# Optimization experiments

Measured on AMD Instinct MI355X. Metric: run time of the kernel, lower is better.

## Reference

```python
import jax, jax.numpy as jnp
import numpy as np

N_WIRES = 3  # state vector of 2^3 = 8 amplitudes, kept as [B,2,2,2]


def _rx(t):
    c = jnp.cos(t / 2); s = jnp.sin(t / 2)
    return jnp.stack([jnp.stack([c + 0j, -1j * s], -1),
                      jnp.stack([-1j * s, c + 0j], -1)], -2).astype(jnp.complex64)


def _ry(t):
    c = jnp.cos(t / 2); s = jnp.sin(t / 2)
    return jnp.stack([jnp.stack([c, -s], -1),
                      jnp.stack([s, c], -1)], -2).astype(jnp.complex64)


def _rz(t):
    e = jnp.exp(-1j * t / 2).astype(jnp.complex64)
    z = jnp.zeros_like(e)
    return jnp.stack([jnp.stack([e, z], -1),
                      jnp.stack([z, jnp.conj(e)], -1)], -2)


def apply_1q(state, mat, wire):
    # state: [B,2,2,2]; mat: [2,2] (shared) or [B,2,2] (per-sample)
    s = jnp.moveaxis(state, 1 + wire, 1)
    sh = s.shape
    s = s.reshape(sh[0], 2, -1)
    m = jnp.broadcast_to(mat, (sh[0], 2, 2))
    s = jnp.einsum('bij,bjk->bik', m, s)
    return jnp.moveaxis(s.reshape(sh), 1, 1 + wire)


def apply_crx(state, t, ctrl, tgt):
    # controlled-RX: apply rx(t) to target subspace where control bit == 1
    mat = _rx(t)  # [2,2]
    s = jnp.moveaxis(state, (1 + ctrl, 1 + tgt), (1, 2))  # [B,2(ctrl),2(tgt),2]
    s1 = s[:, 1]                       # [B,2,2]
    sh = s1.shape
    s1 = jnp.einsum('ij,bjk->bik', mat, s1.reshape(sh[0], 2, -1)).reshape(sh)
    s = jnp.stack([s[:, 0], s1], 1)
    return jnp.moveaxis(s, (1, 2), (1 + ctrl, 1 + tgt))


def _quantum_forward(x, theta, W1, b1, W2, b2):
    B = x.shape[0]
    state = jnp.zeros((B, 2, 2, 2), jnp.complex64).at[:, 0, 0, 0].set(1.0)
    # GeneralEncoder: rx(x0)@w0, ry(x1)@w1, rz(x2)@w2
    state = apply_1q(state, _rx(x[:, 0]), 0)
    state = apply_1q(state, _ry(x[:, 1]), 1)
    state = apply_1q(state, _rz(x[:, 2]), 2)
    # RandomLayer(n_ops=8): fixed representative 8-op trainable sequence
    state = apply_1q(state, _rx(theta[0]), 0)
    state = apply_1q(state, _ry(theta[1]), 1)
    state = apply_1q(state, _rz(theta[2]), 2)
    state = apply_crx(state, theta[3], 0, 1)
    state = apply_1q(state, _ry(theta[4]), 2)
    state = apply_1q(state, _rx(theta[5]), 1)
    state = apply_crx(state, theta[6], 1, 2)
    state = apply_1q(state, _rz(theta[7]), 0)
    # measurement -> 8 basis-state probabilities (matches Linear(8,32) head)
    probs = (state.real ** 2 + state.imag ** 2).reshape(B, 8)
    h = jax.nn.relu(probs @ W1 + b1)
    return h @ W2 + b2


def setup_inputs() -> dict:
    key = jax.random.key(0)
    ks = jax.random.split(key, 6)
    B = 2_000_000
    x = jax.random.normal(ks[0], (B, 3), jnp.float32)
    theta = jax.random.normal(ks[1], (8,), jnp.float32)
    W1 = jax.random.normal(ks[2], (8, 32), jnp.float32) * 0.35   # ~1/sqrt(8)
    b1 = jnp.zeros((32,), jnp.float32)
    W2 = jax.random.normal(ks[3], (32, 2), jnp.float32) * 0.18   # ~1/sqrt(32)
    b2 = jnp.zeros((2,), jnp.float32)
    return {"x": x, "theta": theta, "W1": W1, "b1": b1, "W2": W2, "b2": b2}


def reference(x, theta, W1, b1, W2, b2):
    return _quantum_forward(x, theta, W1, b1, W2, b2)
```

## Files before the change

### kernel.cpp

```cpp
#include <hip/hip_runtime.h>


typedef float f32x2 __attribute__((ext_vector_type(2)));

static __device__ __forceinline__ f32x2 pkfma(f32x2 a, f32x2 b, f32x2 c) {
    f32x2 d;
    asm("v_pk_fma_f32 %0, %1, %2, %3" : "=v"(d) : "v"(a), "v"(b), "v"(c));
    return d;
}
static __device__ __forceinline__ f32x2 pkmul(f32x2 a, f32x2 b) {
    f32x2 d;
    asm("v_pk_mul_f32 %0, %1, %2" : "=v"(d) : "v"(a), "v"(b));
    return d;
}
static __device__ __forceinline__ f32x2 splat2(float v) {
    f32x2 r; r.x = v; r.y = v; return r;
}

#define INV_2PI 0.15915494309189535f

__global__ __launch_bounds__(256, 2) void q_fused(
    const float* __restrict__ x,
    const float* __restrict__ theta,
    const float* __restrict__ W1,
    const float* __restrict__ b1,
    const float* __restrict__ W2,
    const float* __restrict__ b2,
    float* __restrict__ out,
    int B)
{
    __shared__ float Ure[8][8];
    __shared__ float Uim[8][8];
    __shared__ __align__(16) float tab[400];

    const int t = threadIdx.x;

    if (t < 8) {
        float cr[8], ci[8];
        #pragma unroll
        for (int r = 0; r < 8; ++r) { cr[r] = (r == t) ? 1.f : 0.f; ci[r] = 0.f; }

        auto rxmix = [&](int a, int b, float c_, float s_) {
            float ar = cr[a], ai = ci[a], br = cr[b], bi = ci[b];
            cr[a] = c_*ar + s_*bi;   ci[a] = c_*ai - s_*br;
            cr[b] = s_*ai + c_*br;   ci[b] = -s_*ar + c_*bi;
        };
        auto rymix = [&](int a, int b, float c_, float s_) {
            float ar = cr[a], ai = ci[a], br = cr[b], bi = ci[b];
            cr[a] = c_*ar - s_*br;   ci[a] = c_*ai - s_*bi;
            cr[b] = s_*ar + c_*br;   ci[b] = s_*ai + c_*bi;
        };
        auto zmul = [&](int r, float u, float v) {
            float xr = cr[r], xi = ci[r];
            cr[r] = xr*u - xi*v;  ci[r] = xr*v + xi*u;
        };
        auto hsin = [&](float a) { return __builtin_amdgcn_sinf(a * (0.5f*INV_2PI)); };
        auto hcos = [&](float a) { return __builtin_amdgcn_cosf(a * (0.5f*INV_2PI)); };

        float c, s;
        c = hcos(theta[0]); s = hsin(theta[0]);
        rxmix(0,4,c,s); rxmix(1,5,c,s); rxmix(2,6,c,s); rxmix(3,7,c,s);
        c = hcos(theta[1]); s = hsin(theta[1]);
        rymix(0,2,c,s); rymix(1,3,c,s); rymix(4,6,c,s); rymix(5,7,c,s);
        c = hcos(theta[2]); s = hsin(theta[2]);
        #pragma unroll
        for (int r = 0; r < 8; ++r) zmul(r, c, (r & 1) ? s : -s);
        c = hcos(theta[3]); s = hsin(theta[3]);
        rxmix(4,6,c,s); rxmix(5,7,c,s);
        c = hcos(theta[4]); s = hsin(theta[4]);
        rymix(0,1,c,s); rymix(2,3,c,s); rymix(4,5,c,s); rymix(6,7,c,s);
        c = hcos(theta[5]); s = hsin(theta[5]);
        rxmix(0,2,c,s); rxmix(1,3,c,s); rxmix(4,6,c,s); rxmix(5,7,c,s);
        c = hcos(theta[6]); s = hsin(theta[6]);
        rxmix(2,3,c,s); rxmix(6,7,c,s);
        c = hcos(theta[7]); s = hsin(theta[7]);
        #pragma unroll
        for (int r = 0; r < 8; ++r) zmul(r, c, (r < 4) ? -s : s);

        #pragma unroll
        for (int r = 0; r < 8; ++r) { Ure[r][t] = cr[r]; Uim[r][t] = ci[r]; }
    }
    __syncthreads();

    if (t < 32) {
        float Wre[8][4], Wim[8][4];
        #pragma unroll
        for (int j = 0; j < 8; ++j) {
            Wre[j][0] =  Ure[j][0]; Wim[j][0] =  Uim[j][0];
            Wre[j][1] =  Ure[j][2]; Wim[j][1] =  Uim[j][2];
            Wre[j][2] =  Uim[j][4]; Wim[j][2] = -Ure[j][4];
            Wre[j][3] =  Uim[j][6]; Wim[j][3] = -Ure[j][6];
        }
        float Q[4][4];
        #pragma unroll
        for (int m = 0; m < 4; ++m)
            #pragma unroll
            for (int n = 0; n < 4; ++n) Q[m][n] = 0.f;
        #pragma unroll
        for (int j = 0; j < 8; ++j) {
            float w = W1[j*32 + t];
            #pragma unroll
            for (int m = 0; m < 4; ++m)
                #pragma unroll
                for (int n = 0; n < 4; ++n)
                    Q[m][n] = fmaf(w, Wre[j][m]*Wre[j][n] + Wim[j][m]*Wim[j][n], Q[m][n]);
        }
        float R[3][3];
        R[0][0] = Q[0][0];
        R[0][1] = Q[0][1] + Q[1][0];
        R[0][2] = Q[1][1];
        R[1][0] = Q[0][2] + Q[2][0];
        R[1][1] = Q[0][3] + Q[1][2] + Q[2][1] + Q[3][0];
        R[1][2] = Q[1][3] + Q[3][1];
        R[2][0] = Q[2][2];
        R[2][1] = Q[2][3] + Q[3][2];
        R[2][2] = Q[3][3];
        float P[3][3];
        #pragma unroll
        for (int b = 0; b < 3; ++b) {
            P[0][b] = 0.5f*(R[0][b] + R[2][b]);
            P[1][b] = 0.5f*(R[0][b] - R[2][b]);
            P[2][b] = 0.5f*R[1][b];
        }
        float T[3][3];
        #pragma unroll
        for (int si = 0; si < 3; ++si) {
            T[si][0] = 0.5f*(P[si][0] + P[si][2]);
            T[si][1] = 0.5f*(P[si][0] - P[si][2]);
            T[si][2] = 0.5f*P[si][1];
        }
        float* row = tab + t*12;
        row[0] = T[0][1]; row[1] = T[0][2]; row[2] = T[1][0]; row[3] = T[2][0];
        row[4] = T[1][1]; row[5] = T[1][2]; row[6] = T[2][1]; row[7] = T[2][2];
        row[8] = b1[t] + T[0][0];
        row[9]  = W2[t*2+0];
        row[10] = W2[t*2+1];
        row[11] = 0.f;
    }
    if (t == 0) { tab[384] = b2[0]; tab[385] = b2[1]; tab[386] = 0.f; tab[387] = 0.f; }
    __syncthreads();

    const int lid = threadIdx.x;
    const int bb  = blockIdx.x * 2048;
    const int e0  = bb + lid;

    const float b2a = tab[384], b2b = tab[385];
    const float4* T4 = reinterpret_cast<const float4*>(tab);

    float xs0[8], xs1[8];
    #pragma unroll
    for (int k = 0; k < 8; ++k) {
        int e = e0 + k*256;
        e = (e < B) ? e : (B - 1);
        xs0[k] = x[e*3 + 0];
        xs1[k] = x[e*3 + 1];
    }

    f32x2 c0v[4], s0v[4], c1v[4], s1v[4], pcc[4], pcs[4], psc[4], pss[4];
    #pragma unroll
    for (int g = 0; g < 4; ++g) {
        #pragma unroll
        for (int j = 0; j < 2; ++j) {
            const int k = 2*g + j;
            const float r0 = xs0[k] * INV_2PI;
            const float r1 = xs1[k] * INV_2PI;
            s0v[g][j] = __builtin_amdgcn_sinf(r0);
            c0v[g][j] = __builtin_amdgcn_cosf(r0);
            s1v[g][j] = __builtin_amdgcn_sinf(r1);
            c1v[g][j] = __builtin_amdgcn_cosf(r1);
        }
        pcc[g] = pkmul(c0v[g], c1v[g]);
        pcs[g] = pkmul(c0v[g], s1v[g]);
        psc[g] = pkmul(s0v[g], c1v[g]);
        pss[g] = pkmul(s0v[g], s1v[g]);
    }

    f32x2 a0v[4], a1v[4];
    #pragma unroll
    for (int g = 0; g < 4; ++g) { a0v[g] = splat2(b2a); a1v[g] = splat2(b2b); }

    #pragma unroll 2
    for (int l = 0; l < 32; ++l) {
        const float4 cA = T4[l*3+0];
        const float4 cB = T4[l*3+1];
        const float4 cC = T4[l*3+2];
        const f32x2 vb  = splat2(cC.x);
        const f32x2 vA0 = splat2(cA.x), vA1 = splat2(cA.y);
        const f32x2 vA2 = splat2(cA.z), vA3 = splat2(cA.w);
        const f32x2 vB0 = splat2(cB.x), vB1 = splat2(cB.y);
        const f32x2 vB2 = splat2(cB.z), vB3 = splat2(cB.w);
        const f32x2 vw0 = splat2(cC.y), vw1 = splat2(cC.z);
        #pragma unroll
        for (int g = 0; g < 4; ++g) {
            f32x2 h = pkfma(vA0, c1v[g], vb);
            h = pkfma(vA1, s1v[g], h);
            h = pkfma(vA2, c0v[g], h);
            h = pkfma(vA3, s0v[g], h);
            h = pkfma(vB0, pcc[g], h);
            h = pkfma(vB1, pcs[g], h);
            h = pkfma(vB2, psc[g], h);
            h = pkfma(vB3, pss[g], h);
            h = __builtin_elementwise_max(h, splat2(0.f));
            a0v[g] = pkfma(h, vw0, a0v[g]);
            a1v[g] = pkfma(h, vw1, a1v[g]);
        }
    }

    f32x2* O2 = (f32x2*)out;
    #pragma unroll
    for (int k = 0; k < 8; ++k) {
        const int e = e0 + k*256;
        if (e < B) {
            f32x2 o; o.x = a0v[k>>1][k&1]; o.y = a1v[k>>1][k&1];
            O2[e] = o;
        }
    }
}

extern "C" void kernel_launch(void* const* d_in, const int* in_sizes, int n_in,
                              void* d_out, int out_size, void* d_ws, size_t ws_size,
                              hipStream_t stream) {
    const float* x     = (const float*)d_in[0];
    const float* theta = (const float*)d_in[1];
    const float* W1    = (const float*)d_in[2];
    const float* b1    = (const float*)d_in[3];
    const float* W2    = (const float*)d_in[4];
    const float* b2    = (const float*)d_in[5];
    float* out = (float*)d_out;
    (void)d_ws; (void)ws_size;

    const int B = in_sizes[0] / 3;
    const int blocks = (B + 2047) / 2048;
    q_fused<<<blocks, 256, 0, stream>>>(x, theta, W1, b1, W2, b2, out, B);
}
```

Baseline: 100.9 us.

## Split table precompute into separate kernel and feed coefficients via scalar registers

The per-block unitary/quadratic-form precompute moves into a single-block kernel that writes a duplicated-pair coefficient table to workspace. The main kernel then reads the table through uniform loads, so the packed FMAs can take coefficients as SGPR operands instead of splatted VGPRs. The aim is to stop every block from redoing the 8-thread setup and its two barriers, and to cut VGPR use and shared-memory traffic. The cost is an extra kernel launch with a dependency between the two kernels, and it relies on the compiler placing the table loads in scalar registers.

```diff
diff --git a/kernel.cpp b/kernel.cpp
--- a/kernel.cpp
+++ b/kernel.cpp
@@ -3,9 +3,9 @@
 
 typedef float f32x2 __attribute__((ext_vector_type(2)));
 
-static __device__ __forceinline__ f32x2 pkfma(f32x2 a, f32x2 b, f32x2 c) {
+static __device__ __forceinline__ f32x2 pkfma_s(f32x2 coef_s, f32x2 b, f32x2 c) {
     f32x2 d;
-    asm("v_pk_fma_f32 %0, %1, %2, %3" : "=v"(d) : "v"(a), "v"(b), "v"(c));
+    asm("v_pk_fma_f32 %0, %1, %2, %3" : "=v"(d) : "s"(coef_s), "v"(b), "v"(c));
     return d;
 }
 static __device__ __forceinline__ f32x2 pkmul(f32x2 a, f32x2 b) {
@@ -19,20 +19,16 @@
 
 #define INV_2PI 0.15915494309189535f
 
-__global__ __launch_bounds__(256, 2) void q_fused(
-    const float* __restrict__ x,
+__global__ __launch_bounds__(64) void q_precompute(
     const float* __restrict__ theta,
     const float* __restrict__ W1,
     const float* __restrict__ b1,
     const float* __restrict__ W2,
     const float* __restrict__ b2,
-    float* __restrict__ out,
-    int B)
+    float* __restrict__ tab)
 {
     __shared__ float Ure[8][8];
     __shared__ float Uim[8][8];
-    __shared__ __align__(16) float tab[400];
-
     const int t = threadIdx.x;
 
     if (t < 8) {
@@ -129,23 +125,35 @@
             T[si][1] = 0.5f*(P[si][0] - P[si][2]);
             T[si][2] = 0.5f*P[si][1];
         }
-        float* row = tab + t*12;
-        row[0] = T[0][1]; row[1] = T[0][2]; row[2] = T[1][0]; row[3] = T[2][0];
-        row[4] = T[1][1]; row[5] = T[1][2]; row[6] = T[2][1]; row[7] = T[2][2];
-        row[8] = b1[t] + T[0][0];
-        row[9]  = W2[t*2+0];
-        row[10] = W2[t*2+1];
-        row[11] = 0.f;
-    }
-    if (t == 0) { tab[384] = b2[0]; tab[385] = b2[1]; tab[386] = 0.f; tab[387] = 0.f; }
-    __syncthreads();
-
+        float* row = tab + t*24;
+        row[0]  = row[1]  = T[0][1];
+        row[2]  = row[3]  = T[0][2];
+        row[4]  = row[5]  = T[1][0];
+        row[6]  = row[7]  = T[2][0];
+        row[8]  = row[9]  = T[1][1];
+        row[10] = row[11] = T[1][2];
+        row[12] = row[13] = T[2][1];
+        row[14] = row[15] = T[2][2];
+        row[16] = row[17] = b1[t] + T[0][0];
+        row[18] = row[19] = W2[t*2+0];
+        row[20] = row[21] = W2[t*2+1];
+        row[22] = row[23] = 0.f;
+    }
+    if (t == 0) { tab[768] = b2[0]; tab[769] = b2[1]; }
+}
+
+__global__ __launch_bounds__(256) void q_main(
+    const float* __restrict__ x,
+    const float* __restrict__ tab,
+    float* __restrict__ out,
+    int B)
+{
     const int lid = threadIdx.x;
     const int bb  = blockIdx.x * 2048;
     const int e0  = bb + lid;
 
-    const float b2a = tab[384], b2b = tab[385];
-    const float4* T4 = reinterpret_cast<const float4*>(tab);
+    const float b2a = tab[768], b2b = tab[769];
+    const f32x2* Tp = reinterpret_cast<const f32x2*>(tab);
 
     float xs0[8], xs1[8];
     #pragma unroll
@@ -178,31 +186,35 @@
     f32x2 a0v[4], a1v[4];
     #pragma unroll
     for (int g = 0; g < 4; ++g) { a0v[g] = splat2(b2a); a1v[g] = splat2(b2b); }
+    const f32x2 zero2 = splat2(0.f);
 
     #pragma unroll 2
     for (int l = 0; l < 32; ++l) {
-        const float4 cA = T4[l*3+0];
-        const float4 cB = T4[l*3+1];
-        const float4 cC = T4[l*3+2];
-        const f32x2 vb  = splat2(cC.x);
-        const f32x2 vA0 = splat2(cA.x), vA1 = splat2(cA.y);
-        const f32x2 vA2 = splat2(cA.z), vA3 = splat2(cA.w);
-        const f32x2 vB0 = splat2(cB.x), vB1 = splat2(cB.y);
-        const f32x2 vB2 = splat2(cB.z), vB3 = splat2(cB.w);
-        const f32x2 vw0 = splat2(cC.y), vw1 = splat2(cC.z);
+        const int L = l*12;
+        const f32x2 cT01 = Tp[L+0];
+        const f32x2 cT02 = Tp[L+1];
+        const f32x2 cT10 = Tp[L+2];
+        const f32x2 cT20 = Tp[L+3];
+        const f32x2 cT11 = Tp[L+4];
+        const f32x2 cT12 = Tp[L+5];
+        const f32x2 cT21 = Tp[L+6];
+        const f32x2 cT22 = Tp[L+7];
+        const f32x2 cw0  = Tp[L+9];
+        const f32x2 cw1  = Tp[L+10];
+        const f32x2 vb   = splat2(tab[l*24 + 16]);
         #pragma unroll
         for (int g = 0; g < 4; ++g) {
-            f32x2 h = pkfma(vA0, c1v[g], vb);
-            h = pkfma(vA1, s1v[g], h);
-            h = pkfma(vA2, c0v[g], h);
-            h = pkfma(vA3, s0v[g], h);
-            h = pkfma(vB0, pcc[g], h);
-            h = pkfma(vB1, pcs[g], h);
-            h = pkfma(vB2, psc[g], h);
-            h = pkfma(vB3, pss[g], h);
-            h = __builtin_elementwise_max(h, splat2(0.f));
-            a0v[g] = pkfma(h, vw0, a0v[g]);
-            a1v[g] = pkfma(h, vw1, a1v[g]);
+            f32x2 h = pkfma_s(cT01, c1v[g], vb);
+            h = pkfma_s(cT02, s1v[g], h);
+            h = pkfma_s(cT10, c0v[g], h);
+            h = pkfma_s(cT20, s0v[g], h);
+            h = pkfma_s(cT11, pcc[g], h);
+            h = pkfma_s(cT12, pcs[g], h);
+            h = pkfma_s(cT21, psc[g], h);
+            h = pkfma_s(cT22, pss[g], h);
+            h = __builtin_elementwise_max(h, zero2);
+            a0v[g] = pkfma_s(cw0, h, a0v[g]);
+            a1v[g] = pkfma_s(cw1, h, a1v[g]);
         }
     }
 
@@ -227,9 +239,12 @@
     const float* W2    = (const float*)d_in[4];
     const float* b2    = (const float*)d_in[5];
     float* out = (float*)d_out;
-    (void)d_ws; (void)ws_size;
+    float* tab = (float*)d_ws;
 
     const int B = in_sizes[0] / 3;
+
+    q_precompute<<<1, 64, 0, stream>>>(theta, W1, b1, W2, b2, tab);
+
     const int blocks = (B + 2047) / 2048;
-    q_fused<<<blocks, 256, 0, stream>>>(x, theta, W1, b1, W2, b2, out, B);
-}
+    q_main<<<blocks, 256, 0, stream>>>(x, tab, out, B);
+}
```

Result: faster. 98.50 us (-2.4%).
